# Performance work log

Measured on AMD Instinct MI355X. Metric: run time of the kernel, lower is better.

## Reference

```python
import jax, jax.numpy as jnp
import numpy as np

B, N, C = 4, 2048, 768
H = 12
HD = C // H  # 64


def setup_inputs() -> dict:
    key = jax.random.key(0)
    ks = jax.random.split(key, 6)
    s = 0.02
    return {
        "x": jax.random.normal(ks[0], (B, N, C), dtype=jnp.float32),
        "w_qkv": jax.random.normal(ks[1], (C, 3 * C), dtype=jnp.float32) * s,
        "b_qkv": jax.random.normal(ks[2], (3 * C,), dtype=jnp.float32) * s,
        "w_proj": jax.random.normal(ks[3], (C, C), dtype=jnp.float32) * s,
        "b_proj": jax.random.normal(ks[4], (C,), dtype=jnp.float32) * s,
        "key_log_bias": jax.random.normal(ks[5], (B, N), dtype=jnp.float32),
    }


def reference(x, w_qkv, b_qkv, w_proj, b_proj, key_log_bias):
    b, n, c = x.shape
    scale = 1.0 / float(HD) ** 0.5
    qkv = x @ w_qkv + b_qkv                      # [B, N, 3C]
    qkv = qkv.reshape(b, n, 3, H, HD).transpose(2, 0, 3, 1, 4)  # [3, B, H, N, HD]
    q, k, v = qkv[0], qkv[1], qkv[2]
    logits = jnp.einsum('bhqd,bhkd->bhqk', q, k) * scale        # [B, H, N, N]
    logits = logits + key_log_bias[:, None, None, :]            # key-side bias
    attn = jax.nn.softmax(logits, axis=-1)
    out = jnp.einsum('bhqk,bhkd->bhqd', attn, v)                # [B, H, N, HD]
    out = out.transpose(0, 2, 1, 3).reshape(b, n, c)            # [B, N, C]
    return out @ w_proj + b_proj
```

## Files before the change

kernel.cpp:

```cpp
#include <hip/hip_runtime.h>


typedef short short8 __attribute__((ext_vector_type(8)));
typedef float f32x4 __attribute__((ext_vector_type(4)));
typedef unsigned int u32x4 __attribute__((ext_vector_type(4)));

#define GLB_AS(p) ((const __attribute__((address_space(1))) void*)(p))
#define LDS_AS(p) ((__attribute__((address_space(3))) void*)(p))

__device__ __forceinline__ void gload_lds16(const void* g, void* l) {
  __builtin_amdgcn_global_load_lds(GLB_AS(g), LDS_AS(l), 16, 0, 0);
}

__device__ __forceinline__ f32x4 mfma16(short8 a, short8 b, f32x4 c) {
  return __builtin_amdgcn_mfma_f32_16x16x32_bf16(a, b, c, 0, 0, 0);
}

__device__ __forceinline__ unsigned short f2bf(float f) {
  union { float f; unsigned u; } v; v.f = f;
  unsigned r = v.u + 0x7fffu + ((v.u >> 16) & 1u);
  return (unsigned short)(r >> 16);
}

__device__ __forceinline__ float bf2f(unsigned short u) {
  union { unsigned u; float f; } v; v.u = ((unsigned)u) << 16;
  return v.f;
}

__device__ __forceinline__ unsigned cvt_pk_bf16(float a, float b) {
  unsigned r;
  asm("v_cvt_pk_bf16_f32 %0, %1, %2" : "=v"(r) : "v"(a), "v"(b));
  return r;
}

#define LOG2E 1.44269504088896340736f

__device__ __forceinline__ int kappa1(int m) {
  return ((m >> 4) & 1) * 32 + ((m >> 2) & 3) * 8 + ((m >> 5) & 1) * 4 + (m & 3);
}


__global__ __launch_bounds__(256) void cvt_f32_bf16(const float* __restrict__ in,
                                                    unsigned short* __restrict__ out,
                                                    int n8) {
  int i = blockIdx.x * 256 + threadIdx.x;
  if (i >= n8) return;
  const float4* p = (const float4*)in + 2 * (size_t)i;
  float4 a = p[0], c = p[1];
  short8 r;
  r[0] = (short)f2bf(a.x); r[1] = (short)f2bf(a.y); r[2] = (short)f2bf(a.z); r[3] = (short)f2bf(a.w);
  r[4] = (short)f2bf(c.x); r[5] = (short)f2bf(c.y); r[6] = (short)f2bf(c.z); r[7] = (short)f2bf(c.w);
  ((short8*)out)[i] = r;
}

__global__ __launch_bounds__(256) void exp_bias(const float* __restrict__ in,
                                                unsigned short* __restrict__ out, int n) {
  int i = blockIdx.x * 256 + threadIdx.x;
  if (i < n) out[i] = f2bf(__builtin_exp2f(in[i] * LOG2E));
}

__global__ __launch_bounds__(256) void tr_cvt_f32_bf16(const float* __restrict__ src,
                                                       unsigned short* __restrict__ dst,
                                                       int R, int C) {
  __shared__ float t[32][33];
  int tx = threadIdx.x & 31, ty = threadIdx.x >> 5;
  int c0 = blockIdx.x * 32, r0 = blockIdx.y * 32;
#pragma unroll
  for (int i = 0; i < 32; i += 8)
    t[ty + i][tx] = src[(size_t)(r0 + ty + i) * C + c0 + tx];
  __syncthreads();
#pragma unroll
  for (int i = 0; i < 32; i += 8)
    dst[(size_t)(c0 + ty + i) * R + r0 + tx] = f2bf(t[tx][ty + i]);
}

__global__ __launch_bounds__(256) void tr_bf16_head(const unsigned short* __restrict__ src,
                                                    const unsigned short* __restrict__ ebb,
                                                    unsigned short* __restrict__ dst) {
  __shared__ unsigned short t[32][33];
  int tx = threadIdx.x & 31, ty = threadIdx.x >> 5;
  size_t hb = (size_t)blockIdx.z * (2048 * 64);
  int b = blockIdx.z / 12;
  int c0 = blockIdx.x * 32, r0 = blockIdx.y * 32;
#pragma unroll
  for (int i = 0; i < 32; i += 8)
    t[ty + i][tx] = src[hb + (size_t)(r0 + ty + i) * 64 + c0 + tx];
  __syncthreads();
  float eb = bf2f(ebb[b * 2048 + r0 + tx]);
#pragma unroll
  for (int i = 0; i < 32; i += 8)
    dst[hb + (size_t)(c0 + ty + i) * 2048 + r0 + tx] = f2bf(bf2f(t[tx][ty + i]) * eb);
}

template <int EPI>
__global__ __launch_bounds__(256, 2) void gemm_bt(
    const unsigned short* __restrict__ A, const unsigned short* __restrict__ Bt,
    const float* __restrict__ bias, float* __restrict__ outf,
    unsigned short* __restrict__ qo, unsigned short* __restrict__ ko,
    unsigned short* __restrict__ vo, int K) {
  __shared__ __align__(16) unsigned short As[128 * 64];
  __shared__ __align__(16) unsigned short Bs[128 * 64];
  const int tid = threadIdx.x;
  const int lane = tid & 63, wid = tid >> 6;
  const int lr = lane & 15, lg = lane >> 4;
  const int bm = blockIdx.x, bn = blockIdx.y;
  const int wr = (wid >> 1) * 64, wc = (wid & 1) * 64;

  const unsigned short* ap[4];
  const unsigned short* bp[4];
  unsigned loff[4];
#pragma unroll
  for (int i = 0; i < 4; ++i) {
    int c = wid * 4 + i;
    int r = c * 8 + (lane >> 3);
    int gs = (lane & 7) ^ (r & 7);
    ap[i] = A + (size_t)(bm * 128 + r) * K + gs * 8;
    bp[i] = Bt + (size_t)(bn * 128 + r) * K + gs * 8;
    loff[i] = (unsigned)c * 1024;
  }

  f32x4 acc[4][4] = {};
  const int nt = K >> 6;
  for (int t = 0; t < nt; ++t) {
#pragma unroll
    for (int i = 0; i < 4; ++i) {
      gload_lds16(ap[i], (char*)As + loff[i]);
      gload_lds16(bp[i], (char*)Bs + loff[i]);
      ap[i] += 64;
      bp[i] += 64;
    }
    __syncthreads();
#pragma unroll
    for (int kkk = 0; kkk < 2; ++kkk) {
      short8 af[4], bf[4];
#pragma unroll
      for (int mf = 0; mf < 4; ++mf) {
        int r = wr + mf * 16 + lr;
        int g = kkk * 4 + lg;
        af[mf] = *(const short8*)((const char*)As + r * 128 + ((g ^ (r & 7)) << 4));
      }
#pragma unroll
      for (int nf = 0; nf < 4; ++nf) {
        int r = wc + nf * 16 + lr;
        int g = kkk * 4 + lg;
        bf[nf] = *(const short8*)((const char*)Bs + r * 128 + ((g ^ (r & 7)) << 4));
      }
#pragma unroll
      for (int mf = 0; mf < 4; ++mf)
#pragma unroll
        for (int nf = 0; nf < 4; ++nf)
          acc[mf][nf] = mfma16(af[mf], bf[nf], acc[mf][nf]);
    }
    __syncthreads();
  }

  const int colbase = bn * 128 + wc;
  float bv[4];
#pragma unroll
  for (int nf = 0; nf < 4; ++nf) bv[nf] = bias[colbase + nf * 16 + lr];

  if constexpr (EPI == 0) {
#pragma unroll
    for (int nf = 0; nf < 4; ++nf) {
      int col = colbase + nf * 16 + lr;
      int which = col / 768;
      int rem = col - which * 768;
      int h = rem >> 6, d = rem & 63;
#pragma unroll
      for (int mf = 0; mf < 4; ++mf) {
#pragma unroll
        for (int j = 0; j < 4; ++j) {
          int row = bm * 128 + wr + mf * 16 + lg * 4 + j;
          int bb = row >> 11, nn = row & 2047;
          float v = acc[mf][nf][j] + bv[nf];
          size_t off = (((size_t)bb * 12 + h) * 2048 + nn) * 64 + d;
          if (which == 0)
            qo[off] = f2bf(v * (0.125f * LOG2E));
          else if (which == 1)
            ko[off] = f2bf(v);
          else
            vo[off] = f2bf(v);
        }
      }
    }
  } else {
#pragma unroll
    for (int mf = 0; mf < 4; ++mf) {
#pragma unroll
      for (int j = 0; j < 4; ++j) {
        int row = bm * 128 + wr + mf * 16 + lg * 4 + j;
#pragma unroll
        for (int nf = 0; nf < 4; ++nf) {
          int col = colbase + nf * 16 + lr;
          outf[(size_t)row * 768 + col] = acc[mf][nf][j] + bv[nf];
        }
      }
    }
  }
}

__global__ __launch_bounds__(256, 3) void attn_fused(
    const unsigned short* __restrict__ Q, const unsigned short* __restrict__ Kx,
    const unsigned short* __restrict__ Vt, const unsigned short* __restrict__ ebb,
    unsigned short* __restrict__ Ao) {
  __shared__ __align__(16) unsigned short Ks[2][64 * 64];
  __shared__ __align__(16) unsigned short Vs[2][64 * 64];
  const int tid = threadIdx.x, lane = tid & 63, wid = tid >> 6;
  const int lr = lane & 15, lg = lane >> 4;
  const int qb = blockIdx.x, bh = blockIdx.y;
  const int b = bh / 12, h = bh - b * 12;
  const size_t hoff = (size_t)bh * (2048 * 64);
  const unsigned short* Qh = Q + hoff;
  const unsigned short* Kh = Kx + hoff;
  const unsigned short* Vh = Vt + hoff;
  const unsigned short* ebh = ebb + b * 2048;

  short8 qf[2][2];
#pragma unroll
  for (int mf = 0; mf < 2; ++mf)
#pragma unroll
    for (int kkk = 0; kkk < 2; ++kkk) {
      int qr = qb * 128 + wid * 32 + mf * 16 + lr;
      qf[mf][kkk] = *(const short8*)(Qh + (size_t)qr * 64 + kkk * 32 + lg * 8);
    }

  const int c0 = wid * 2, c1 = wid * 2 + 1;
  const int r0s = c0 * 8 + (lane >> 3), r1s = c1 * 8 + (lane >> 3);
  const int g0 = (lane & 7) ^ (r0s & 7), g1 = (lane & 7) ^ (r1s & 7);
  const int k1r0 = kappa1(r0s), k1r1 = kappa1(r1s);

  unsigned koff[2][4], voff[2][4];
#pragma unroll
  for (int kkk = 0; kkk < 2; ++kkk)
#pragma unroll
    for (int nf = 0; nf < 4; ++nf) {
      int r = nf * 16 + lr, g = kkk * 4 + lg;
      koff[kkk][nf] = (unsigned)(r * 128 + ((g ^ (r & 7)) << 4));
      voff[kkk][nf] = koff[kkk][nf];
    }

  f32x4 o[2][4] = {};
  f32x4 ol[2] = {};

#define STAGE(buf, t)                                                                  \
  do {                                                                                 \
    const int kt0_ = (t) * 64;                                                         \
    gload_lds16(Kh + (size_t)(kt0_ + k1r0) * 64 + g0 * 8, (char*)Ks[buf] + c0 * 1024); \
    gload_lds16(Kh + (size_t)(kt0_ + k1r1) * 64 + g1 * 8, (char*)Ks[buf] + c1 * 1024); \
    gload_lds16(Vh + (size_t)r0s * 2048 + kt0_ + g0 * 8, (char*)Vs[buf] + c0 * 1024);  \
    gload_lds16(Vh + (size_t)r1s * 2048 + kt0_ + g1 * 8, (char*)Vs[buf] + c1 * 1024);  \
  } while (0)

#define BODY(buf, kt0)                                                                 \
  do {                                                                                 \
    short8 ebf[2];                                                                     \
    _Pragma("unroll") for (int kkk = 0; kkk < 2; ++kkk)                                \
        ebf[kkk] = *(const short8*)(ebh + (kt0) + kkk * 32 + lg * 8);                  \
    f32x4 s[4][2] = {};                                                                \
    _Pragma("unroll") for (int kkk = 0; kkk < 2; ++kkk) {                              \
      short8 kf[4];                                                                    \
      _Pragma("unroll") for (int nf = 0; nf < 4; ++nf)                                 \
          kf[nf] = *(const short8*)((const char*)Ks[buf] + koff[kkk][nf]);             \
      _Pragma("unroll") for (int nf = 0; nf < 4; ++nf)                                 \
          _Pragma("unroll") for (int mf = 0; mf < 2; ++mf)                             \
              s[nf][mf] = mfma16(kf[nf], qf[mf][kkk], s[nf][mf]);                      \
    }                                                                                  \
    _Pragma("unroll") for (int nf = 0; nf < 4; ++nf)                                   \
        _Pragma("unroll") for (int mf = 0; mf < 2; ++mf)                               \
            _Pragma("unroll") for (int j = 0; j < 4; ++j)                              \
                s[nf][mf][j] = __builtin_exp2f(s[nf][mf][j]);                          \
    short8 pa[2][2];                                                                   \
    _Pragma("unroll") for (int mf = 0; mf < 2; ++mf)                                   \
        _Pragma("unroll") for (int kkk = 0; kkk < 2; ++kkk) {                          \
      u32x4 w;                                                                         \
      w[0] = cvt_pk_bf16(s[kkk][mf][0], s[kkk][mf][1]);                                \
      w[1] = cvt_pk_bf16(s[kkk][mf][2], s[kkk][mf][3]);                                \
      w[2] = cvt_pk_bf16(s[kkk + 2][mf][0], s[kkk + 2][mf][1]);                        \
      w[3] = cvt_pk_bf16(s[kkk + 2][mf][2], s[kkk + 2][mf][3]);                        \
      pa[mf][kkk] = __builtin_bit_cast(short8, w);                                     \
    }                                                                                  \
    _Pragma("unroll") for (int kkk = 0; kkk < 2; ++kkk) {                              \
      short8 vf[4];                                                                    \
      _Pragma("unroll") for (int nf = 0; nf < 4; ++nf)                                 \
          vf[nf] = *(const short8*)((const char*)Vs[buf] + voff[kkk][nf]);             \
      _Pragma("unroll") for (int mf = 0; mf < 2; ++mf) {                               \
        ol[mf] = mfma16(pa[mf][kkk], ebf[kkk], ol[mf]);                                \
        _Pragma("unroll") for (int nf = 0; nf < 4; ++nf)                               \
            o[mf][nf] = mfma16(pa[mf][kkk], vf[nf], o[mf][nf]);                        \
      }                                                                                \
    }                                                                                  \
  } while (0)

  STAGE(0, 0);

  for (int t = 0; t < 32; t += 2) {
    __syncthreads();
    STAGE(1, t + 1);
    BODY(0, t * 64);
    __syncthreads();
    if (t + 2 < 32) STAGE(0, t + 2);
    BODY(1, (t + 1) * 64);
  }
#undef STAGE
#undef BODY

#pragma unroll
  for (int mf = 0; mf < 2; ++mf)
#pragma unroll
    for (int j = 0; j < 4; ++j) {
      float inv = 1.f / ol[mf][j];
      int qr = qb * 128 + wid * 32 + mf * 16 + lg * 4 + j;
#pragma unroll
      for (int nf = 0; nf < 4; ++nf) {
        int d = nf * 16 + lr;
        Ao[((size_t)b * 2048 + qr) * 768 + h * 64 + d] = f2bf(o[mf][nf][j] * inv);
      }
    }
}


extern "C" void kernel_launch(void* const* d_in, const int* in_sizes, int n_in,
                              void* d_out, int out_size, void* d_ws, size_t ws_size,
                              hipStream_t stream) {
  (void)in_sizes; (void)n_in; (void)out_size; (void)ws_size;
  const float* x = (const float*)d_in[0];
  const float* wqkv = (const float*)d_in[1];
  const float* bqkv = (const float*)d_in[2];
  const float* wproj = (const float*)d_in[3];
  const float* bproj = (const float*)d_in[4];
  const float* klb = (const float*)d_in[5];
  float* out = (float*)d_out;
  char* ws = (char*)d_ws;

  const size_t SZ = (size_t)8192 * 768 * 2;
  unsigned short* xb = (unsigned short*)(ws);
  unsigned short* wqkvT = (unsigned short*)(ws + SZ);
  unsigned short* wprojT = (unsigned short*)(ws + SZ + 3538944);
  unsigned short* qbuf = (unsigned short*)(ws + SZ + 3538944 + 1179648);
  unsigned short* kbuf = (unsigned short*)(ws + SZ + 3538944 + 1179648 + SZ);
  unsigned short* vbuf = (unsigned short*)(ws + SZ + 3538944 + 1179648 + 2 * SZ);
  unsigned short* vtbuf = (unsigned short*)(ws + SZ + 3538944 + 1179648 + 3 * SZ);
  unsigned short* ebb = (unsigned short*)(ws + SZ + 3538944 + 1179648 + 4 * SZ);
  unsigned short* aob = xb;

  cvt_f32_bf16<<<dim3(3072), dim3(256), 0, stream>>>(x, xb, 786432);
  exp_bias<<<dim3(32), dim3(256), 0, stream>>>(klb, ebb, 8192);
  tr_cvt_f32_bf16<<<dim3(72, 24), dim3(256), 0, stream>>>(wqkv, wqkvT, 768, 2304);
  tr_cvt_f32_bf16<<<dim3(24, 24), dim3(256), 0, stream>>>(wproj, wprojT, 768, 768);
  gemm_bt<0><<<dim3(64, 18), dim3(256), 0, stream>>>(xb, wqkvT, bqkv, nullptr,
                                                     qbuf, kbuf, vbuf, 768);
  tr_bf16_head<<<dim3(2, 64, 48), dim3(256), 0, stream>>>(vbuf, ebb, vtbuf);
  attn_fused<<<dim3(16, 48), dim3(256), 0, stream>>>(qbuf, kbuf, vtbuf, ebb, aob);
  gemm_bt<1><<<dim3(64, 6), dim3(256), 0, stream>>>(aob, wprojT, bproj, out,
                                                    nullptr, nullptr, nullptr, 768);
}
```

Measured before the change: 155.7 us.

## Merge prep kernels into one launch and fuse V transpose into QKV epilogue

Four preprocessing kernels (x conversion, exp of key bias, and two weight transposes) are combined into a single launch that dispatches on block index. The separate V transpose-and-bias-scale kernel is removed. The QKV GEMM epilogue now writes V already transposed and multiplied by exp(key bias). This drops launch overhead and a full round trip of V through memory, at the cost of strided, uncoalesced 2-byte stores for V in the GEMM epilogue.

```diff
diff --git a/kernel.cpp b/kernel.cpp
--- a/kernel.cpp
+++ b/kernel.cpp
@@ -39,32 +39,40 @@
   return ((m >> 4) & 1) * 32 + ((m >> 2) & 3) * 8 + ((m >> 5) & 1) * 4 + (m & 3);
 }
 
-
-__global__ __launch_bounds__(256) void cvt_f32_bf16(const float* __restrict__ in,
-                                                    unsigned short* __restrict__ out,
-                                                    int n8) {
-  int i = blockIdx.x * 256 + threadIdx.x;
-  if (i >= n8) return;
-  const float4* p = (const float4*)in + 2 * (size_t)i;
-  float4 a = p[0], c = p[1];
-  short8 r;
-  r[0] = (short)f2bf(a.x); r[1] = (short)f2bf(a.y); r[2] = (short)f2bf(a.z); r[3] = (short)f2bf(a.w);
-  r[4] = (short)f2bf(c.x); r[5] = (short)f2bf(c.y); r[6] = (short)f2bf(c.z); r[7] = (short)f2bf(c.w);
-  ((short8*)out)[i] = r;
-}
-
-__global__ __launch_bounds__(256) void exp_bias(const float* __restrict__ in,
-                                                unsigned short* __restrict__ out, int n) {
-  int i = blockIdx.x * 256 + threadIdx.x;
-  if (i < n) out[i] = f2bf(__builtin_exp2f(in[i] * LOG2E));
-}
-
-__global__ __launch_bounds__(256) void tr_cvt_f32_bf16(const float* __restrict__ src,
-                                                       unsigned short* __restrict__ dst,
-                                                       int R, int C) {
+__global__ __launch_bounds__(256) void prep(
+    const float* __restrict__ x, unsigned short* __restrict__ xb,
+    const float* __restrict__ klb, unsigned short* __restrict__ ebb,
+    const float* __restrict__ wqkv, unsigned short* __restrict__ wqkvT,
+    const float* __restrict__ wproj, unsigned short* __restrict__ wprojT) {
+  const int bid = blockIdx.x, tid = threadIdx.x;
+  if (bid < 3072) {
+    int i = bid * 256 + tid;
+    const float4* p = (const float4*)x + 2 * (size_t)i;
+    float4 a = p[0], c = p[1];
+    short8 r;
+    r[0] = (short)f2bf(a.x); r[1] = (short)f2bf(a.y); r[2] = (short)f2bf(a.z); r[3] = (short)f2bf(a.w);
+    r[4] = (short)f2bf(c.x); r[5] = (short)f2bf(c.y); r[6] = (short)f2bf(c.z); r[7] = (short)f2bf(c.w);
+    ((short8*)xb)[i] = r;
+    return;
+  }
+  if (bid < 3104) {
+    int i = (bid - 3072) * 256 + tid;
+    ebb[i] = f2bf(__builtin_exp2f(klb[i] * LOG2E));
+    return;
+  }
   __shared__ float t[32][33];
-  int tx = threadIdx.x & 31, ty = threadIdx.x >> 5;
-  int c0 = blockIdx.x * 32, r0 = blockIdx.y * 32;
+  const float* src;
+  unsigned short* dst;
+  int R, C, bx, by;
+  if (bid < 4832) {
+    int i = bid - 3104;
+    src = wqkv; dst = wqkvT; R = 768; C = 2304; bx = i % 72; by = i / 72;
+  } else {
+    int i = bid - 4832;
+    src = wproj; dst = wprojT; R = 768; C = 768; bx = i % 24; by = i / 24;
+  }
+  int tx = tid & 31, ty = tid >> 5;
+  int c0 = bx * 32, r0 = by * 32;
 #pragma unroll
   for (int i = 0; i < 32; i += 8)
     t[ty + i][tx] = src[(size_t)(r0 + ty + i) * C + c0 + tx];
@@ -72,24 +80,6 @@
 #pragma unroll
   for (int i = 0; i < 32; i += 8)
     dst[(size_t)(c0 + ty + i) * R + r0 + tx] = f2bf(t[tx][ty + i]);
-}
-
-__global__ __launch_bounds__(256) void tr_bf16_head(const unsigned short* __restrict__ src,
-                                                    const unsigned short* __restrict__ ebb,
-                                                    unsigned short* __restrict__ dst) {
-  __shared__ unsigned short t[32][33];
-  int tx = threadIdx.x & 31, ty = threadIdx.x >> 5;
-  size_t hb = (size_t)blockIdx.z * (2048 * 64);
-  int b = blockIdx.z / 12;
-  int c0 = blockIdx.x * 32, r0 = blockIdx.y * 32;
-#pragma unroll
-  for (int i = 0; i < 32; i += 8)
-    t[ty + i][tx] = src[hb + (size_t)(r0 + ty + i) * 64 + c0 + tx];
-  __syncthreads();
-  float eb = bf2f(ebb[b * 2048 + r0 + tx]);
-#pragma unroll
-  for (int i = 0; i < 32; i += 8)
-    dst[hb + (size_t)(c0 + ty + i) * 2048 + r0 + tx] = f2bf(bf2f(t[tx][ty + i]) * eb);
 }
 
 template <int EPI>
@@ -97,7 +87,8 @@
     const unsigned short* __restrict__ A, const unsigned short* __restrict__ Bt,
     const float* __restrict__ bias, float* __restrict__ outf,
     unsigned short* __restrict__ qo, unsigned short* __restrict__ ko,
-    unsigned short* __restrict__ vo, int K) {
+    unsigned short* __restrict__ vo, const unsigned short* __restrict__ ebb,
+    int K) {
   __shared__ __align__(16) unsigned short As[128 * 64];
   __shared__ __align__(16) unsigned short Bs[128 * 64];
   const int tid = threadIdx.x;
@@ -173,13 +164,14 @@
           int row = bm * 128 + wr + mf * 16 + lg * 4 + j;
           int bb = row >> 11, nn = row & 2047;
           float v = acc[mf][nf][j] + bv[nf];
-          size_t off = (((size_t)bb * 12 + h) * 2048 + nn) * 64 + d;
-          if (which == 0)
-            qo[off] = f2bf(v * (0.125f * LOG2E));
-          else if (which == 1)
-            ko[off] = f2bf(v);
-          else
-            vo[off] = f2bf(v);
+          if (which == 0) {
+            qo[(((size_t)bb * 12 + h) * 2048 + nn) * 64 + d] = f2bf(v * (0.125f * LOG2E));
+          } else if (which == 1) {
+            ko[(((size_t)bb * 12 + h) * 2048 + nn) * 64 + d] = f2bf(v);
+          } else {
+            float eb = bf2f(ebb[bb * 2048 + nn]);
+            vo[(((size_t)bb * 12 + h) * 64 + d) * 2048 + nn] = f2bf(v * eb);
+          }
         }
       }
     }
@@ -338,19 +330,16 @@
   unsigned short* wprojT = (unsigned short*)(ws + SZ + 3538944);
   unsigned short* qbuf = (unsigned short*)(ws + SZ + 3538944 + 1179648);
   unsigned short* kbuf = (unsigned short*)(ws + SZ + 3538944 + 1179648 + SZ);
-  unsigned short* vbuf = (unsigned short*)(ws + SZ + 3538944 + 1179648 + 2 * SZ);
-  unsigned short* vtbuf = (unsigned short*)(ws + SZ + 3538944 + 1179648 + 3 * SZ);
-  unsigned short* ebb = (unsigned short*)(ws + SZ + 3538944 + 1179648 + 4 * SZ);
+  unsigned short* vtbuf = (unsigned short*)(ws + SZ + 3538944 + 1179648 + 2 * SZ);
+  unsigned short* ebb = (unsigned short*)(ws + SZ + 3538944 + 1179648 + 3 * SZ);
   unsigned short* aob = xb;
 
-  cvt_f32_bf16<<<dim3(3072), dim3(256), 0, stream>>>(x, xb, 786432);
-  exp_bias<<<dim3(32), dim3(256), 0, stream>>>(klb, ebb, 8192);
-  tr_cvt_f32_bf16<<<dim3(72, 24), dim3(256), 0, stream>>>(wqkv, wqkvT, 768, 2304);
-  tr_cvt_f32_bf16<<<dim3(24, 24), dim3(256), 0, stream>>>(wproj, wprojT, 768, 768);
+  prep<<<dim3(5408), dim3(256), 0, stream>>>(x, xb, klb, ebb, wqkv, wqkvT,
+                                             wproj, wprojT);
   gemm_bt<0><<<dim3(64, 18), dim3(256), 0, stream>>>(xb, wqkvT, bqkv, nullptr,
-                                                     qbuf, kbuf, vbuf, 768);
-  tr_bf16_head<<<dim3(2, 64, 48), dim3(256), 0, stream>>>(vbuf, ebb, vtbuf);
+                                                     qbuf, kbuf, vtbuf, ebb, 768);
   attn_fused<<<dim3(16, 48), dim3(256), 0, stream>>>(qbuf, kbuf, vtbuf, ebb, aob);
   gemm_bt<1><<<dim3(64, 6), dim3(256), 0, stream>>>(aob, wprojT, bproj, out,
-                                                    nullptr, nullptr, nullptr, 768);
-}
+                                                    nullptr, nullptr, nullptr,
+                                                    nullptr, 768);
+}
```

Measured after the change: 161.1 us. 3.4% more time.
